# Kernel optimization log

Hardware: AMD Instinct MI355X
Metric: run time of the kernel (lower is better)

## Reference

```python
import jax, jax.numpy as jnp
import numpy as np

N = 50000      # nodes
E2 = 400000    # undirected edges
E = 2 * E2     # directed edges (each undirected edge in both directions)
DIN = 512      # input feature dim
DH = 128       # MLP hidden
C = 8          # num classes / BP channels


def setup_inputs() -> dict:
    key = jax.random.key(0)
    ks = jax.random.split(key, 9)
    x = jax.random.normal(ks[0], (N, DIN), jnp.float32)
    src0 = jax.random.randint(ks[1], (E2,), 0, N)
    dst0 = jax.random.randint(ks[2], (E2,), 0, N)
    # symmetric directed edge list: row 0 = source j, row 1 = target i
    edge_index = jnp.stack([jnp.concatenate([src0, dst0]),
                            jnp.concatenate([dst0, src0])])
    w0 = jax.random.uniform(ks[3], (E2,), jnp.float32, 0.5, 1.5)
    edge_weight = jnp.concatenate([w0, w0])  # reverse edge shares weight
    # edge_rv[e] = index of the reverse of edge e
    edge_rv = jnp.concatenate([jnp.arange(E2) + E2, jnp.arange(E2)])
    W1 = jax.random.normal(ks[4], (DIN, DH), jnp.float32) * 0.05
    b1 = jnp.zeros((DH,), jnp.float32)
    W2 = jax.random.normal(ks[5], (DH, C), jnp.float32) * 0.05
    b2 = jnp.zeros((C,), jnp.float32)
    param = jax.random.normal(ks[6], (C, C), jnp.float32) * 0.1
    return {"x": x, "edge_index": edge_index, "edge_weight": edge_weight,
            "edge_rv": edge_rv, "W1": W1, "b1": b1, "W2": W2, "b2": b2,
            "param": param, "K": 5}


def log_normalize(log_x):
    return log_x - jax.nn.logsumexp(log_x, axis=-1, keepdims=True)


def reference(x, edge_index, edge_weight, edge_rv, W1, b1, W2, b2, param, K):
    # MLP transform + LogSoftmax -> initial log-beliefs [N, C]
    h = jax.nn.relu(x @ W1 + b1)
    log_b0 = jax.nn.log_softmax(h @ W2 + b2, axis=-1)

    # learn_H=True: logH = logsigmoid(param + param^T), [C, C]
    logH = jax.nn.log_sigmoid(param + param.T)
    src, dst = edge_index[0], edge_index[1]
    # per-edge coupling matrix [E, C, C]
    logC = edge_weight[:, None, None] * logH[None, :, :]

    log_b = log_b0
    log_msg = None
    for _ in range(K):
        x_j = log_b[src]                       # gather source beliefs [E, C]
        if log_msg is not None:
            x_j = x_j - log_msg[edge_rv]       # remove reverse message
        # tropical-semiring matvec in log domain: logsumexp over source channel
        log_msg = log_normalize(jax.nn.logsumexp(x_j[:, :, None] + logC, axis=1))
        agg = jax.ops.segment_sum(log_msg, dst, num_segments=N)  # scatter-add
        log_b = log_normalize(log_b0 + agg)
    return log_b
```

## Files before the change

kernel.cpp:

```cpp
#include <hip/hip_runtime.h>
#include <hip/hip_bf16.h>
#include <hip/hip_fp16.h>
#include <math.h>

#define NN 50000
#define EE 800000
#define E2K 400000
#define DINK 512
#define DHK 128
#define CK 8
#define KIT 5
#define NBLKS 196

typedef __attribute__((ext_vector_type(8))) short short8;
typedef __attribute__((ext_vector_type(4))) float f32x4;

__device__ __forceinline__ unsigned short f2bf(float f) {
    union { float f; unsigned int u; } v;
    v.f = f;
    unsigned int u = v.u;
    unsigned int r = (u + 0x7FFFu + ((u >> 16) & 1u)) >> 16;
    return (unsigned short)r;
}
__device__ __forceinline__ float bfu2f(unsigned int lo16) {
    union { unsigned int u; float f; } v;
    v.u = lo16 << 16;
    return v.f;
}

__global__ __launch_bounds__(256) void prep_kernel(
    const float* __restrict__ W1, const float* __restrict__ param,
    unsigned short* __restrict__ W1t, float* __restrict__ logH) {
    if (blockIdx.x < 256) {
        int idx = blockIdx.x * 256 + threadIdx.x;
        int n = idx >> 9;
        int k = idx & 511;
        W1t[idx] = f2bf(W1[(size_t)k * DHK + n]);
    } else if (threadIdx.x < 64) {
        int t = threadIdx.x;
        int i = t >> 3, j = t & 7;
        float z = param[i * 8 + j] + param[j * 8 + i];
        logH[t] = fminf(z, 0.0f) - log1pf(expf(-fabsf(z)));
    }
}

__global__ __launch_bounds__(256) void mlp_mfma_kernel(
    const float* __restrict__ x, const unsigned short* __restrict__ W1t,
    const float* __restrict__ b1, const float* __restrict__ W2,
    const float* __restrict__ b2, float* __restrict__ logb0) {
    __shared__ unsigned short hs[128 * 136];
    __shared__ float W2s[128 * 8];
    __shared__ float b1s[128];
    __shared__ float b2s[8];

    const int tid = threadIdx.x;
    const int wave = tid >> 6;
    const int lane = tid & 63;
    const int q = lane >> 4;
    const int lm = lane & 15;
    const int wm = wave >> 1, wn = wave & 1;
    const int n0 = blockIdx.x * 128;

    if (tid < 128) b1s[tid] = b1[tid];
    if (tid < 8) b2s[tid] = b2[tid];
    {
        int i = tid * 4;
        *(float4*)&W2s[i] = *(const float4*)&W2[i];
    }
    __syncthreads();

    const float* xptr[4];
#pragma unroll
    for (int mt = 0; mt < 4; ++mt) {
        int r = n0 + wm * 64 + mt * 16 + lm;
        if (r > NN - 1) r = NN - 1;
        xptr[mt] = x + (size_t)r * DINK + q * 8;
    }
    const unsigned short* bptr[4];
#pragma unroll
    for (int nt = 0; nt < 4; ++nt) {
        int c = wn * 64 + nt * 16 + lm;
        bptr[nt] = W1t + (size_t)c * DINK + q * 8;
    }

    f32x4 acc[4][4];
#pragma unroll
    for (int mt = 0; mt < 4; ++mt)
#pragma unroll
        for (int nt = 0; nt < 4; ++nt) acc[mt][nt] = (f32x4){0.f, 0.f, 0.f, 0.f};

    float4 ar[4][2];
    short8 bc[4];
#pragma unroll
    for (int mt = 0; mt < 4; ++mt) {
        ar[mt][0] = *(const float4*)(xptr[mt]);
        ar[mt][1] = *(const float4*)(xptr[mt] + 4);
    }
#pragma unroll
    for (int nt = 0; nt < 4; ++nt) bc[nt] = *(const short8*)(bptr[nt]);

#pragma unroll
    for (int k0 = 32; k0 <= DINK; k0 += 32) {
        float4 ar2[4][2];
        short8 b2f[4];
        if (k0 < DINK) {
#pragma unroll
            for (int mt = 0; mt < 4; ++mt) {
                ar2[mt][0] = *(const float4*)(xptr[mt] + k0);
                ar2[mt][1] = *(const float4*)(xptr[mt] + k0 + 4);
            }
#pragma unroll
            for (int nt = 0; nt < 4; ++nt)
                b2f[nt] = *(const short8*)(bptr[nt] + k0);
        }
        short8 af[4];
#pragma unroll
        for (int mt = 0; mt < 4; ++mt) {
            union { short8 s; __hip_bfloat162 h[4]; } cv;
            cv.h[0] = __float22bfloat162_rn(make_float2(ar[mt][0].x, ar[mt][0].y));
            cv.h[1] = __float22bfloat162_rn(make_float2(ar[mt][0].z, ar[mt][0].w));
            cv.h[2] = __float22bfloat162_rn(make_float2(ar[mt][1].x, ar[mt][1].y));
            cv.h[3] = __float22bfloat162_rn(make_float2(ar[mt][1].z, ar[mt][1].w));
            af[mt] = cv.s;
        }
#pragma unroll
        for (int mt = 0; mt < 4; ++mt)
#pragma unroll
            for (int nt = 0; nt < 4; ++nt)
                acc[mt][nt] = __builtin_amdgcn_mfma_f32_16x16x32_bf16(
                    af[mt], bc[nt], acc[mt][nt], 0, 0, 0);
        if (k0 < DINK) {
#pragma unroll
            for (int mt = 0; mt < 4; ++mt) {
                ar[mt][0] = ar2[mt][0];
                ar[mt][1] = ar2[mt][1];
            }
#pragma unroll
            for (int nt = 0; nt < 4; ++nt) bc[nt] = b2f[nt];
        }
    }

#pragma unroll
    for (int nt = 0; nt < 4; ++nt) {
        int j = wn * 64 + nt * 16 + lm;
        float bj = b1s[j];
#pragma unroll
        for (int mt = 0; mt < 4; ++mt) {
            int rbase = wm * 64 + mt * 16 + q * 4;
#pragma unroll
            for (int r = 0; r < 4; ++r) {
                float h = fmaxf(acc[mt][nt][r] + bj, 0.0f);
                hs[(rbase + r) * 136 + j] = f2bf(h);
            }
        }
    }
    __syncthreads();

    int row = tid >> 1;
    int half = tid & 1;
    const unsigned short* hp = &hs[row * 136 + half * 64];
    float p[8] = {0.f, 0.f, 0.f, 0.f, 0.f, 0.f, 0.f, 0.f};
#pragma unroll
    for (int ch = 0; ch < 8; ++ch) {
        uint4 c4 = *(const uint4*)(hp + ch * 8);
        unsigned int uu[4] = {c4.x, c4.y, c4.z, c4.w};
#pragma unroll
        for (int p2 = 0; p2 < 4; ++p2) {
            float h0 = bfu2f(uu[p2] & 0xFFFFu);
            float h1 = bfu2f(uu[p2] >> 16);
            int j = half * 64 + ch * 8 + p2 * 2;
            const float* w0 = &W2s[j * 8];
            const float* w1 = &W2s[(j + 1) * 8];
#pragma unroll
            for (int c = 0; c < 8; ++c) p[c] = fmaf(h0, w0[c], p[c]);
#pragma unroll
            for (int c = 0; c < 8; ++c) p[c] = fmaf(h1, w1[c], p[c]);
        }
    }
#pragma unroll
    for (int c = 0; c < 8; ++c) p[c] += __shfl_xor(p[c], 1, 64);
    int grow = n0 + row;
    if (half == 0 && grow < NN) {
        float v[8];
        float mx = -1e30f;
#pragma unroll
        for (int c = 0; c < 8; ++c) {
            v[c] = p[c] + b2s[c];
            mx = fmaxf(mx, v[c]);
        }
        float s = 0.0f;
#pragma unroll
        for (int c = 0; c < 8; ++c) s += expf(v[c] - mx);
        float ln = mx + logf(s);
        float4* p0 = (float4*)&logb0[(size_t)grow * 8];
        p0[0] = make_float4(v[0] - ln, v[1] - ln, v[2] - ln, v[3] - ln);
        p0[1] = make_float4(v[4] - ln, v[5] - ln, v[6] - ln, v[7] - ln);
    }
}


__global__ __launch_bounds__(256) void deg_pair_kernel(const int* __restrict__ ei,
                                                       int* __restrict__ cnt) {
    int e = blockIdx.x * 256 + threadIdx.x;
    if (e >= E2K) return;
    int s = ei[e];
    int d = ei[EE + e];
    atomicAdd(&cnt[d], 1);
    atomicAdd(&cnt[s], 1);
}

__global__ __launch_bounds__(256) void scan_partial_kernel(
    const int* __restrict__ cnt, int* __restrict__ partial) {
    __shared__ int sd[256];
    int t = threadIdx.x;
    int i = blockIdx.x * 256 + t;
    sd[t] = (i < NN) ? cnt[i] : 0;
    __syncthreads();
#pragma unroll
    for (int s = 128; s > 0; s >>= 1) {
        if (t < s) sd[t] += sd[t + s];
        __syncthreads();
    }
    if (t == 0) partial[blockIdx.x] = sd[0];
}

__global__ __launch_bounds__(256) void scan_tops_kernel(
    const int* __restrict__ partial, int* __restrict__ tops) {
    __shared__ int sd[256];
    int t = threadIdx.x;
    sd[t] = (t < NBLKS) ? partial[t] : 0;
    __syncthreads();
#pragma unroll
    for (int s = 1; s < 256; s <<= 1) {
        int a = sd[t];
        int b = (t >= s) ? sd[t - s] : 0;
        __syncthreads();
        sd[t] = a + b;
        __syncthreads();
    }
    if (t < NBLKS) tops[t] = (t > 0) ? sd[t - 1] : 0;
}

__global__ __launch_bounds__(256) void scan_write_kernel(
    const int* __restrict__ cnt, const int* __restrict__ tops,
    int* __restrict__ off) {
    __shared__ int sd[256];
    int t = threadIdx.x;
    int i = blockIdx.x * 256 + t;
    int v = (i < NN) ? cnt[i] : 0;
    sd[t] = v;
    __syncthreads();
#pragma unroll
    for (int s = 1; s < 256; s <<= 1) {
        int a = sd[t];
        int b = (t >= s) ? sd[t - s] : 0;
        __syncthreads();
        sd[t] = a + b;
        __syncthreads();
    }
    if (i < NN) off[i] = tops[blockIdx.x] + sd[t] - v;
    if (i == NN - 1) off[NN] = EE;
}

__global__ __launch_bounds__(256) void pos_pair_kernel(
    const int* __restrict__ ei, const float* __restrict__ ew,
    const int* __restrict__ off, int* __restrict__ cnt,
    int2* __restrict__ perm_sw, int* __restrict__ rvp) {
    int e = blockIdx.x * 256 + threadIdx.x;
    if (e >= E2K) return;
    int s = ei[e];
    int d = ei[EE + e];
    int wbits = __float_as_int(ew[e]);
    int pA = off[d] + atomicAdd(&cnt[d], 1);
    int pB = off[s] + atomicAdd(&cnt[s], 1);
    int2 v;
    v.x = s; v.y = wbits; perm_sw[pA] = v;
    v.x = d;              perm_sw[pB] = v;
    rvp[pA] = pB;
    rvp[pB] = pA;
}

__global__ __launch_bounds__(256) void msg_kernel(
    const int2* __restrict__ perm_sw, const int* __restrict__ rvp,
    const float* __restrict__ logH, const uint4* __restrict__ msg_prev,
    const float* __restrict__ bel_prev, uint4* __restrict__ msg_next,
    int first) {
    __shared__ float lH[64];
    const int t = threadIdx.x;
    if (t < 64) lH[t] = logH[t];
    __syncthreads();

    const int base = blockIdx.x * 512 + t;
    int jj[2];
    int2 sw[2];
#pragma unroll
    for (int e = 0; e < 2; ++e) {
        int j = base + e * 256;
        jj[e] = j;
        int jc = (j < EE) ? j : (EE - 1);
        sw[e] = perm_sw[jc];
    }
    float4 ba[2], bb[2];
#pragma unroll
    for (int e = 0; e < 2; ++e) {
        const float4* pb = (const float4*)&bel_prev[(size_t)sw[e].x * 8];
        ba[e] = pb[0];
        bb[e] = pb[1];
    }
    uint4 mp[2];
    if (!first) {
        int rv[2];
#pragma unroll
        for (int e = 0; e < 2; ++e) {
            int j = jj[e];
            int jc = (j < EE) ? j : (EE - 1);
            rv[e] = rvp[jc];
        }
#pragma unroll
        for (int e = 0; e < 2; ++e) mp[e] = msg_prev[rv[e]];
    }

#pragma unroll
    for (int e = 0; e < 2; ++e) {
        float w = __int_as_float(sw[e].y);
        float xj[8];
        xj[0] = ba[e].x; xj[1] = ba[e].y; xj[2] = ba[e].z; xj[3] = ba[e].w;
        xj[4] = bb[e].x; xj[5] = bb[e].y; xj[6] = bb[e].z; xj[7] = bb[e].w;
        if (!first) {
            union { uint4 u; _Float16 h[8]; } cv;
            cv.u = mp[e];
#pragma unroll
            for (int k = 0; k < 8; ++k) xj[k] -= (float)cv.h[k];
        }
        float M = xj[0];
#pragma unroll
        for (int k = 1; k < 8; ++k) M = fmaxf(M, xj[k]);
#pragma unroll
        for (int k = 0; k < 8; ++k) xj[k] -= M;
        float mg[8];
#pragma unroll
        for (int c2 = 0; c2 < 8; ++c2) {
            float ssum = 0.0f;
#pragma unroll
            for (int c1 = 0; c1 < 8; ++c1)
                ssum += __expf(fmaf(w, lH[c1 * 8 + c2], xj[c1]));
            mg[c2] = __logf(ssum);
        }
        float mm = mg[0];
#pragma unroll
        for (int k = 1; k < 8; ++k) mm = fmaxf(mm, mg[k]);
        float se = 0.0f;
#pragma unroll
        for (int k = 0; k < 8; ++k) se += __expf(mg[k] - mm);
        float ln = mm + __logf(se);
        union { uint4 u; _Float16 h[8]; } ov;
#pragma unroll
        for (int k = 0; k < 8; ++k) ov.h[k] = (_Float16)(mg[k] - ln);
        if (jj[e] < EE) msg_next[jj[e]] = ov.u;
    }
}

__global__ __launch_bounds__(256) void agg_kernel(
    const float* __restrict__ logb0, const int* __restrict__ off,
    const uint4* __restrict__ msg, float* __restrict__ bel_next,
    float* __restrict__ out, int last) {
    const int t = threadIdx.x;
    const int n = blockIdx.x * 32 + (t >> 3);
    const int c = t & 7;
    if (n >= NN) return;
    float a = logb0[(size_t)n * 8 + c];
    const int j0 = off[n];
    const int j1 = off[n + 1];
    const _Float16* mh = (const _Float16*)msg;
    for (int j = j0; j < j1; ++j) a += (float)mh[(size_t)j * 8 + c];
    float mx = a;
#pragma unroll
    for (int s = 1; s < 8; s <<= 1) mx = fmaxf(mx, __shfl_xor(mx, s, 8));
    float sum = __expf(a - mx);
#pragma unroll
    for (int s = 1; s < 8; s <<= 1) sum += __shfl_xor(sum, s, 8);
    float v = a - (mx + __logf(sum));
    if (last) out[(size_t)n * 8 + c] = v;
    else bel_next[(size_t)n * 8 + c] = v;
}

extern "C" void kernel_launch(void* const* d_in, const int* in_sizes, int n_in,
                              void* d_out, int out_size, void* d_ws, size_t ws_size,
                              hipStream_t stream) {
    const float* x = (const float*)d_in[0];
    const int* ei = (const int*)d_in[1];
    const float* ew = (const float*)d_in[2];
    const float* W1 = (const float*)d_in[4];
    const float* b1 = (const float*)d_in[5];
    const float* W2 = (const float*)d_in[6];
    const float* b2 = (const float*)d_in[7];
    const float* param = (const float*)d_in[8];
    float* out = (float*)d_out;

    float* wsf = (float*)d_ws;
    float* logH = wsf;
    float* logb0 = logH + 64;
    uint4* msgA = (uint4*)(logb0 + (size_t)NN * 8);
    uint4* msgB = msgA + EE;
    int* off = (int*)(msgB + EE);
    int2* perm_sw = (int2*)(off + 50004);
    int* rvp = (int*)(perm_sw + EE);
    unsigned short* W1t = (unsigned short*)(rvp + EE);
    float* belA = (float*)(W1t + 65536);
    float* belB = belA + (size_t)NN * 8;
    int* cnt = (int*)msgA;
    int* partial = cnt + NN;
    int* tops = partial + NBLKS;

    prep_kernel<<<257, 256, 0, stream>>>(W1, param, W1t, logH);
    mlp_mfma_kernel<<<(NN + 127) / 128, 256, 0, stream>>>(x, W1t, b1, W2, b2,
                                                          logb0);

    const int E2B = (E2K + 255) / 256;

    hipMemsetAsync(cnt, 0, (size_t)NN * sizeof(int), stream);
    deg_pair_kernel<<<E2B, 256, 0, stream>>>(ei, cnt);
    scan_partial_kernel<<<NBLKS, 256, 0, stream>>>(cnt, partial);
    scan_tops_kernel<<<1, 256, 0, stream>>>(partial, tops);
    scan_write_kernel<<<NBLKS, 256, 0, stream>>>(cnt, tops, off);
    hipMemsetAsync(cnt, 0, (size_t)NN * sizeof(int), stream);
    pos_pair_kernel<<<E2B, 256, 0, stream>>>(ei, ew, off, cnt, perm_sw, rvp);

    const int MB = (EE + 511) / 512;
    const int AB = (NN + 31) / 32;
    uint4* msgs[2] = {msgA, msgB};
    float* bels[2] = {belA, belB};
    const float* bprev = logb0;
    for (int it = 0; it < KIT; ++it) {
        msg_kernel<<<MB, 256, 0, stream>>>(
            perm_sw, rvp, logH, msgs[(it + 1) & 1] , bprev,
            msgs[it & 1] , it == 0 ? 1 : 0);
        agg_kernel<<<AB, 256, 0, stream>>>(
            logb0, off, msgs[it & 1], bels[it & 1], out,
            it == KIT - 1 ? 1 : 0);
        bprev = bels[it & 1];
    }
}
```

Measured before the change: 463.4 us.

## Drop per-edge message normalization, prefetch 4 edges per thread, fold memsets

The message kernel no longer subtracts the max or log-normalizes each message. Any per-edge constant shift is removed later when the beliefs are log-normalized, so this cuts exp/log work per edge. Each thread now handles four edges, loading the next edge's belief and reverse message while computing the current one. The two count-clearing memsets are folded into the prep and scan_write kernels, and the aggregation loop uses four independent accumulators. Messages are now stored unnormalized in fp16, and exps are taken without max subtraction, which risks range or precision loss.

```diff
diff --git a/kernel.cpp b/kernel.cpp
--- a/kernel.cpp
+++ b/kernel.cpp
@@ -11,6 +11,7 @@
 #define CK 8
 #define KIT 5
 #define NBLKS 196
+#define EPT 4
 
 typedef __attribute__((ext_vector_type(8))) short short8;
 typedef __attribute__((ext_vector_type(4))) float f32x4;
@@ -30,17 +31,23 @@
 
 __global__ __launch_bounds__(256) void prep_kernel(
     const float* __restrict__ W1, const float* __restrict__ param,
-    unsigned short* __restrict__ W1t, float* __restrict__ logH) {
+    unsigned short* __restrict__ W1t, float* __restrict__ logH,
+    int* __restrict__ cnt) {
     if (blockIdx.x < 256) {
         int idx = blockIdx.x * 256 + threadIdx.x;
         int n = idx >> 9;
         int k = idx & 511;
         W1t[idx] = f2bf(W1[(size_t)k * DHK + n]);
-    } else if (threadIdx.x < 64) {
-        int t = threadIdx.x;
-        int i = t >> 3, j = t & 7;
-        float z = param[i * 8 + j] + param[j * 8 + i];
-        logH[t] = fminf(z, 0.0f) - log1pf(expf(-fabsf(z)));
+    } else if (blockIdx.x == 256) {
+        if (threadIdx.x < 64) {
+            int t = threadIdx.x;
+            int i = t >> 3, j = t & 7;
+            float z = param[i * 8 + j] + param[j * 8 + i];
+            logH[t] = fminf(z, 0.0f) - log1pf(expf(-fabsf(z)));
+        }
+    } else {
+        int i = (blockIdx.x - 257) * 256 + threadIdx.x;
+        if (i < NN) cnt[i] = 0;
     }
 }
 
@@ -243,7 +250,7 @@
 
 __global__ __launch_bounds__(256) void scan_write_kernel(
     const int* __restrict__ cnt, const int* __restrict__ tops,
-    int* __restrict__ off) {
+    int* __restrict__ off, int* __restrict__ cnt_z) {
     __shared__ int sd[256];
     int t = threadIdx.x;
     int i = blockIdx.x * 256 + t;
@@ -258,7 +265,10 @@
         sd[t] = a + b;
         __syncthreads();
     }
-    if (i < NN) off[i] = tops[blockIdx.x] + sd[t] - v;
+    if (i < NN) {
+        off[i] = tops[blockIdx.x] + sd[t] - v;
+        cnt_z[i] = 0;
+    }
     if (i == NN - 1) off[NN] = EE;
 }
 
@@ -290,53 +300,47 @@
     if (t < 64) lH[t] = logH[t];
     __syncthreads();
 
-    const int base = blockIdx.x * 512 + t;
-    int jj[2];
-    int2 sw[2];
-#pragma unroll
-    for (int e = 0; e < 2; ++e) {
+    const int base = blockIdx.x * (256 * EPT) + t;
+
+    int jj[EPT];
+    int2 sw[EPT];
+    int rv[EPT];
+#pragma unroll
+    for (int e = 0; e < EPT; ++e) {
         int j = base + e * 256;
         jj[e] = j;
         int jc = (j < EE) ? j : (EE - 1);
         sw[e] = perm_sw[jc];
-    }
-    float4 ba[2], bb[2];
-#pragma unroll
-    for (int e = 0; e < 2; ++e) {
-        const float4* pb = (const float4*)&bel_prev[(size_t)sw[e].x * 8];
-        ba[e] = pb[0];
-        bb[e] = pb[1];
-    }
-    uint4 mp[2];
-    if (!first) {
-        int rv[2];
-#pragma unroll
-        for (int e = 0; e < 2; ++e) {
-            int j = jj[e];
-            int jc = (j < EE) ? j : (EE - 1);
-            rv[e] = rvp[jc];
-        }
-#pragma unroll
-        for (int e = 0; e < 2; ++e) mp[e] = msg_prev[rv[e]];
-    }
-
-#pragma unroll
-    for (int e = 0; e < 2; ++e) {
+        rv[e] = rvp[jc];
+    }
+
+    const float* pb0 = &bel_prev[(size_t)sw[0].x * 8];
+    float4 ba = *(const float4*)pb0;
+    float4 bb = *(const float4*)(pb0 + 4);
+    uint4 mp = make_uint4(0, 0, 0, 0);
+    if (!first) mp = msg_prev[rv[0]];
+
+#pragma unroll
+    for (int e = 0; e < EPT; ++e) {
+        float4 nba = ba, nbb = bb;
+        uint4 nmp = mp;
+        if (e + 1 < EPT) {
+            const float* pb = &bel_prev[(size_t)sw[e + 1].x * 8];
+            nba = *(const float4*)pb;
+            nbb = *(const float4*)(pb + 4);
+            if (!first) nmp = msg_prev[rv[e + 1]];
+        }
+
         float w = __int_as_float(sw[e].y);
         float xj[8];
-        xj[0] = ba[e].x; xj[1] = ba[e].y; xj[2] = ba[e].z; xj[3] = ba[e].w;
-        xj[4] = bb[e].x; xj[5] = bb[e].y; xj[6] = bb[e].z; xj[7] = bb[e].w;
+        xj[0] = ba.x; xj[1] = ba.y; xj[2] = ba.z; xj[3] = ba.w;
+        xj[4] = bb.x; xj[5] = bb.y; xj[6] = bb.z; xj[7] = bb.w;
         if (!first) {
             union { uint4 u; _Float16 h[8]; } cv;
-            cv.u = mp[e];
+            cv.u = mp;
 #pragma unroll
             for (int k = 0; k < 8; ++k) xj[k] -= (float)cv.h[k];
         }
-        float M = xj[0];
-#pragma unroll
-        for (int k = 1; k < 8; ++k) M = fmaxf(M, xj[k]);
-#pragma unroll
-        for (int k = 0; k < 8; ++k) xj[k] -= M;
         float mg[8];
 #pragma unroll
         for (int c2 = 0; c2 < 8; ++c2) {
@@ -346,17 +350,12 @@
                 ssum += __expf(fmaf(w, lH[c1 * 8 + c2], xj[c1]));
             mg[c2] = __logf(ssum);
         }
-        float mm = mg[0];
-#pragma unroll
-        for (int k = 1; k < 8; ++k) mm = fmaxf(mm, mg[k]);
-        float se = 0.0f;
-#pragma unroll
-        for (int k = 0; k < 8; ++k) se += __expf(mg[k] - mm);
-        float ln = mm + __logf(se);
         union { uint4 u; _Float16 h[8]; } ov;
 #pragma unroll
-        for (int k = 0; k < 8; ++k) ov.h[k] = (_Float16)(mg[k] - ln);
+        for (int k = 0; k < 8; ++k) ov.h[k] = (_Float16)mg[k];
         if (jj[e] < EE) msg_next[jj[e]] = ov.u;
+
+        ba = nba; bb = nbb; mp = nmp;
     }
 }
 
@@ -372,7 +371,16 @@
     const int j0 = off[n];
     const int j1 = off[n + 1];
     const _Float16* mh = (const _Float16*)msg;
-    for (int j = j0; j < j1; ++j) a += (float)mh[(size_t)j * 8 + c];
+    float s0 = 0.f, s1 = 0.f, s2 = 0.f, s3 = 0.f;
+    int j = j0;
+    for (; j + 4 <= j1; j += 4) {
+        s0 += (float)mh[(size_t)(j + 0) * 8 + c];
+        s1 += (float)mh[(size_t)(j + 1) * 8 + c];
+        s2 += (float)mh[(size_t)(j + 2) * 8 + c];
+        s3 += (float)mh[(size_t)(j + 3) * 8 + c];
+    }
+    for (; j < j1; ++j) s0 += (float)mh[(size_t)j * 8 + c];
+    a += (s0 + s1) + (s2 + s3);
     float mx = a;
 #pragma unroll
     for (int s = 1; s < 8; s <<= 1) mx = fmaxf(mx, __shfl_xor(mx, s, 8));
@@ -412,21 +420,19 @@
     int* partial = cnt + NN;
     int* tops = partial + NBLKS;
 
-    prep_kernel<<<257, 256, 0, stream>>>(W1, param, W1t, logH);
+    prep_kernel<<<257 + NBLKS, 256, 0, stream>>>(W1, param, W1t, logH, cnt);
     mlp_mfma_kernel<<<(NN + 127) / 128, 256, 0, stream>>>(x, W1t, b1, W2, b2,
                                                           logb0);
 
     const int E2B = (E2K + 255) / 256;
 
-    hipMemsetAsync(cnt, 0, (size_t)NN * sizeof(int), stream);
     deg_pair_kernel<<<E2B, 256, 0, stream>>>(ei, cnt);
     scan_partial_kernel<<<NBLKS, 256, 0, stream>>>(cnt, partial);
     scan_tops_kernel<<<1, 256, 0, stream>>>(partial, tops);
-    scan_write_kernel<<<NBLKS, 256, 0, stream>>>(cnt, tops, off);
-    hipMemsetAsync(cnt, 0, (size_t)NN * sizeof(int), stream);
+    scan_write_kernel<<<NBLKS, 256, 0, stream>>>(cnt, tops, off, cnt);
     pos_pair_kernel<<<E2B, 256, 0, stream>>>(ei, ew, off, cnt, perm_sw, rvp);
 
-    const int MB = (EE + 511) / 512;
+    const int MB = (EE + 256 * EPT - 1) / (256 * EPT);
     const int AB = (NN + 31) / 32;
     uint4* msgs[2] = {msgA, msgB};
     float* bels[2] = {belA, belB};
```

New measurement: 441.4 us. 4.7% less time.
